# Kernel tuning notes

Measured on AMD Instinct MI355X. Metric: run time of the kernel, lower is better.

## Reference

```python
import jax, jax.numpy as jnp
import numpy as np

N = 32768          # total nodes in batch (M graphs * N_agents)
E = N * 8          # edges (k_neighbors = 8)
DIN = 16           # node_obs_dim
DE = 8             # edge_dim (rel_pos 2 + one-hot 4 + dist 1 + payoff 1)
HE = 128           # embed_hidden_size
C = 64             # TransformerConv out_channels
H = 4              # heads (concat)
HC = H * C         # 256, final node embedding dim
EPS = 1e-5


def _ln(x, g, b):
    m = x.mean(-1, keepdims=True)
    v = ((x - m) ** 2).mean(-1, keepdims=True)
    return (x - m) * jax.lax.rsqrt(v + EPS) * g + b


def _seg_softmax(s, seg, n):
    # numerically stable softmax over edges grouped by destination node
    m = jax.ops.segment_max(s, seg, num_segments=n)
    e = jnp.exp(s - m[seg])
    z = jax.ops.segment_sum(e, seg, num_segments=n)
    return e / z[seg]


def setup_inputs() -> dict:
    key = jax.random.key(0)
    ks = jax.random.split(key, 40)

    def w(i, shape):
        return jax.random.normal(ks[i], shape, jnp.float32) * 0.05

    inp = {
        "x": jax.random.normal(ks[0], (N, DIN), jnp.float32),
        "edge_index": jax.random.randint(ks[1], (2, E), 0, N, dtype=jnp.int32),
        "edge_attr": jax.random.normal(ks[2], (E, DE), jnp.float32),
        # EmbedConv: lin1 + LN + one hidden Linear + LN (embed_layer_N=1)
        "e_W1": w(3, (DIN + DE, HE)), "e_b1": jnp.zeros((HE,), jnp.float32),
        "e_g1": jnp.ones((HE,), jnp.float32), "e_be1": jnp.zeros((HE,), jnp.float32),
        "e_W2": w(4, (HE, HE)), "e_b2": jnp.zeros((HE,), jnp.float32),
        "e_g2": jnp.ones((HE,), jnp.float32), "e_be2": jnp.zeros((HE,), jnp.float32),
    }
    # Two TransformerConv layers; layer0 in=HE, layer1 in=HC (concat heads)
    for l, din in enumerate([HE, HC]):
        base = 5 + l * 6
        inp[f"l{l}_Wq"] = w(base, (din, HC));     inp[f"l{l}_bq"] = jnp.zeros((HC,), jnp.float32)
        inp[f"l{l}_Wk"] = w(base + 1, (din, HC)); inp[f"l{l}_bk"] = jnp.zeros((HC,), jnp.float32)
        inp[f"l{l}_Wv"] = w(base + 2, (din, HC)); inp[f"l{l}_bv"] = jnp.zeros((HC,), jnp.float32)
        inp[f"l{l}_We"] = w(base + 3, (DE, HC))   # lin_edge has no bias in PyG
        inp[f"l{l}_Ws"] = w(base + 4, (din, HC)); inp[f"l{l}_bs"] = jnp.zeros((HC,), jnp.float32)
    return inp


def _tconv(h, edge_attr, src, dst, Wq, bq, Wk, bk, Wv, bv, We, Ws, bs):
    q = (h @ Wq + bq).reshape(N, H, C)
    k = (h @ Wk + bk).reshape(N, H, C)
    v = (h @ Wv + bv).reshape(N, H, C)
    e = (edge_attr @ We).reshape(E, H, C)
    ke = k[src] + e                      # [E,H,C]
    ve = v[src] + e                      # [E,H,C]
    s = (q[dst] * ke).sum(-1) / np.float32(np.sqrt(C))  # [E,H]
    a = _seg_softmax(s, dst, N)          # softmax over in-edges of each dst
    out = jax.ops.segment_sum(a[..., None] * ve, dst, num_segments=N)
    return out.reshape(N, HC) + h @ Ws + bs  # root_weight skip + bias


def reference(x, edge_attr, e_W1, e_b1, e_g1, e_be1, e_W2, e_b2, e_g2, e_be2,
              l0_Wq, l0_bq, l0_Wk, l0_bk, l0_Wv, l0_bv, l0_We, l0_Ws, l0_bs,
              l1_Wq, l1_bq, l1_Wk, l1_bk, l1_Wv, l1_bv, l1_We, l1_Ws, l1_bs,
              edge_index):
    src, dst = edge_index[0], edge_index[1]
    # EmbedConv: per-edge MLP on cat(x_j, edge_attr), scatter-add to dst
    m = jnp.concatenate([x[src], edge_attr], axis=1)    # [E, DIN+DE]
    m = _ln(jax.nn.relu(m @ e_W1 + e_b1), e_g1, e_be1)
    m = _ln(jax.nn.relu(m @ e_W2 + e_b2), e_g2, e_be2)
    h = jax.ops.segment_sum(m, dst, num_segments=N)      # [N, HE]
    # Two TransformerConv layers with ReLU activations
    h = jax.nn.relu(_tconv(h, edge_attr, src, dst, l0_Wq, l0_bq, l0_Wk, l0_bk,
                           l0_Wv, l0_bv, l0_We, l0_Ws, l0_bs))
    h = jax.nn.relu(_tconv(h, edge_attr, src, dst, l1_Wq, l1_bq, l1_Wk, l1_bk,
                           l1_Wv, l1_bv, l1_We, l1_Ws, l1_bs))
    return h  # graph_aggr == 'node': [N, HC]
```

## Files before the change

### kernel.cpp

```cpp
#include <hip/hip_runtime.h>
#include <hip/hip_bf16.h>

#define NN 32768
#define NE 262144

typedef unsigned short u16;
typedef unsigned int   u32;
typedef __bf16 bf16x8 __attribute__((ext_vector_type(8)));
typedef float  f32x16 __attribute__((ext_vector_type(16)));

__device__ __forceinline__ float bf2f(u16 u){ return __uint_as_float(((u32)u)<<16); }
__device__ __forceinline__ u16 f2bf(float f){ __hip_bfloat16 h = __float2bfloat16(f); return *(u16*)&h; }
__device__ __forceinline__ float4 ldbf4(const u16* p){
  ushort4 u = *(const ushort4*)p;
  return make_float4(bf2f(u.x), bf2f(u.y), bf2f(u.z), bf2f(u.w));
}
__device__ __forceinline__ void gload16(const void* g, void* l){
  __builtin_amdgcn_global_load_lds(
      (const __attribute__((address_space(1))) void*)g,
      (__attribute__((address_space(3))) void*)l, 16, 0, 0);
}

__global__ void k_deg(const int* __restrict__ ei, int* deg){
  int e = blockIdx.x*256 + threadIdx.x;
  if (e < NE) atomicAdd(&deg[ei[NE + e]], 1);
}

__global__ void k_scan1(const int* __restrict__ deg, int* __restrict__ rowptr, int* __restrict__ bsum){
  const int t = threadIdx.x, b = blockIdx.x;
  const int i = b*256 + t;
  const int ln = t & 63, wv = t >> 6;
  int v = deg[i];
  #pragma unroll
  for (int d = 1; d < 64; d <<= 1){
    int u = __shfl_up(v, d, 64);
    if (ln >= d) v += u;
  }
  __shared__ int wsum[4];
  if (ln == 63) wsum[wv] = v;
  __syncthreads();
  int p = 0;
  #pragma unroll
  for (int w = 0; w < 4; w++) if (w < wv) p += wsum[w];
  v += p;
  rowptr[i + 1] = v;
  if (t == 255) bsum[b] = v;
}

__global__ void k_scan2(const int* __restrict__ bsum, int* __restrict__ boff){
  const int t = threadIdx.x;
  const int ln = t & 63, wv = t >> 6;
  int own = bsum[t];
  int v = own;
  #pragma unroll
  for (int d = 1; d < 64; d <<= 1){
    int u = __shfl_up(v, d, 64);
    if (ln >= d) v += u;
  }
  __shared__ int wsum[2];
  if (ln == 63) wsum[wv] = v;
  __syncthreads();
  if (wv == 1) v += wsum[0];
  boff[t] = v - own;
}

__global__ void k_scan3(int* __restrict__ rowptr, const int* __restrict__ boff){
  const int t = threadIdx.x, b = blockIdx.x;
  rowptr[1 + b*256 + t] += boff[b];
  if (b == 0 && t == 0) rowptr[0] = 0;
}

__global__ void k_fill(const int* __restrict__ ei, const int* __restrict__ rowptr,
                       int* cursor, const float* __restrict__ ea,
                       int* __restrict__ csrc, float4* __restrict__ ea_csr){
  int e = blockIdx.x*256 + threadIdx.x;
  if (e < NE){
    int d = ei[NE + e];
    int p = rowptr[d] + atomicAdd(&cursor[d], 1);
    csrc[p] = ei[e];
    float4 a = *(const float4*)&ea[(size_t)e*8];
    float4 b = *(const float4*)&ea[(size_t)e*8 + 4];
    ea_csr[(size_t)p*2]     = a;
    ea_csr[(size_t)p*2 + 1] = b;
  }
}

__global__ void k_b2p(const float* __restrict__ W2, const float* __restrict__ be1,
                      const float* __restrict__ b2, float* __restrict__ b2p){
  int f = threadIdx.x;
  float a = b2[f];
  for (int k = 0; k < 128; k++) a += be1[k]*W2[k*128 + f];
  b2p[f] = a;
}

__global__ void k_eprep(const float* __restrict__ W1, const float* __restrict__ b1,
                        const float* __restrict__ W2, const float* __restrict__ g1,
                        const float* __restrict__ b2p, __bf16* __restrict__ Ecat){
  int i = blockIdx.x*256 + threadIdx.x;
  if (i >= 2816) return;
  bf16x8 v;
  if (i < 512){
    int r = i & 31, hh = (i>>5)&1, ks = (i>>6)&1, rt = i>>7;
    int feat = rt*32 + r, k0 = ks*16 + hh*8;
    #pragma unroll
    for (int j = 0; j < 8; j++){
      int k = k0 + j;
      float val = (k < 24) ? W1[k*128 + feat] : ((k == 24) ? b1[feat] : 0.f);
      v[j] = (__bf16)val;
    }
  } else {
    int m = i - 512;
    int r = m & 31, hh = (m>>5)&1, q = m>>6;
    int ks = q % 9, rt = q / 9;
    int feat = rt*32 + r, k0 = ks*16 + hh*8;
    #pragma unroll
    for (int j = 0; j < 8; j++){
      int k = k0 + j;
      float val = (k < 128) ? g1[k]*W2[k*128 + feat] : ((k == 128) ? b2p[feat] : 0.f);
      v[j] = (__bf16)val;
    }
  }
  *(bf16x8*)&Ecat[(size_t)i*8] = v;
}

struct WPtrs { const float* w[8]; const float* b[8]; };

__global__ void k_wprep(WPtrs wp, __bf16* __restrict__ W0cat, __bf16* __restrict__ W1cat,
                        float* __restrict__ bcat0, float* __restrict__ bcat1){
  int gid = blockIdx.x*256 + threadIdx.x;
  if (gid < 16384){
    int mat = gid >> 12, v = gid & 4095;
    int colm = v & 255, q = v >> 8;
    int k0 = (q>>1)*16 + (q&1)*8;
    const float* W = wp.w[mat];
    bf16x8 vec;
    #pragma unroll
    for (int j = 0; j < 8; j++) vec[j] = (__bf16)W[(size_t)(k0+j)*256 + colm];
    *(bf16x8*)&W0cat[((size_t)q*1024 + mat*256 + colm)*8] = vec;
  } else if (gid < 49152){
    int g = gid - 16384;
    int mat = g >> 13, v = g & 8191;
    int colm = v & 255, q = v >> 8;
    int k0 = (q>>1)*16 + (q&1)*8;
    const float* W = wp.w[4+mat];
    bf16x8 vec;
    #pragma unroll
    for (int j = 0; j < 8; j++) vec[j] = (__bf16)W[(size_t)(k0+j)*256 + colm];
    *(bf16x8*)&W1cat[((size_t)q*1024 + mat*256 + colm)*8] = vec;
  } else if (gid < 51200){
    int g = gid - 49152;
    if (g < 1024) bcat0[g] = wp.b[g>>8][g&255];
    else { int h = g-1024; bcat1[h] = wp.b[4 + (h>>8)][h&255]; }
  }
}

__global__ __launch_bounds__(256, 1) void k_embed(
    const float* __restrict__ x, const float4* __restrict__ ea_csr,
    const int* __restrict__ csrc, const int* __restrict__ rowptr,
    const __bf16* __restrict__ Ecat,
    const float* __restrict__ g2, const float* __restrict__ be2,
    u16* __restrict__ h0b)
{
  __shared__ alignas(16) __bf16 sE[2816*8];
  __shared__ float sg2[128], sbe2[128];
  const int t = threadIdx.x;
  const int wv = t >> 6, ln = t & 63, hi = ln >> 5, c32 = ln & 31;

  #pragma unroll
  for (int k = 0; k < 11; k++){
    int base = k*256 + wv*64;
    gload16(Ecat + (size_t)(base + ln)*8, &sE[(size_t)base*8]);
  }
  if (t < 128){ sg2[t] = g2[t]; sbe2[t] = be2[t]; }
  asm volatile("s_waitcnt vmcnt(0)" ::: "memory");
  __syncthreads();

  const int d   = (blockIdx.x*4 + wv)*32 + c32;
  const int rp  = rowptr[d];
  const int deg = rowptr[d+1] - rp;
  int md = deg;
  #pragma unroll
  for (int m = 1; m < 32; m <<= 1) md = max(md, __shfl_xor(md, m, 32));

  f32x16 hacc[4] = {};

  bool vc = deg > 0;
  int p0 = vc ? rp : 0;
  int sc = csrc[p0];
  float4 xa = *(const float4*)&x[(size_t)sc*16 + hi*8];
  float4 xb = *(const float4*)&x[(size_t)sc*16 + hi*8 + 4];
  float4 ga = ea_csr[(size_t)p0*2];
  float4 gb = ea_csr[(size_t)p0*2 + 1];

  for (int j = 0; j < md; j++){
    const float vm = vc ? 1.f : 0.f;
    bf16x8 b1f0, b1f1;
    {
      float xv[8]; *(float4*)&xv[0] = xa; *(float4*)&xv[4] = xb;
      #pragma unroll
      for (int q = 0; q < 8; q++) b1f0[q] = (__bf16)(xv[q]*vm);
      float evv[8]; *(float4*)&evv[0] = ga; *(float4*)&evv[4] = gb;
      #pragma unroll
      for (int q = 0; q < 8; q++)
        b1f1[q] = (__bf16)(hi ? ((q == 0) ? vm : 0.f) : evv[q]*vm);
    }

    bool vn = (j + 1) < deg;
    int pn = vn ? (rp + j + 1) : 0;
    int sn = csrc[pn];
    float4 xan = *(const float4*)&x[(size_t)sn*16 + hi*8];
    float4 xbn = *(const float4*)&x[(size_t)sn*16 + hi*8 + 4];
    float4 gan = ea_csr[(size_t)pn*2];
    float4 gbn = ea_csr[(size_t)pn*2 + 1];

    f32x16 a1[4] = {};
    #pragma unroll
    for (int ks = 0; ks < 2; ks++)
      #pragma unroll
      for (int rt = 0; rt < 4; rt++){
        bf16x8 af = *(const bf16x8*)&sE[((((rt*2 + ks)*2 + hi)*32) + c32)*8];
        a1[rt] = __builtin_amdgcn_mfma_f32_32x32x16_bf16(af, ks ? b1f1 : b1f0, a1[rt], 0, 0, 0);
      }

    {
      float s1 = 0.f, s2 = 0.f;
      #pragma unroll
      for (int rt = 0; rt < 4; rt++)
        #pragma unroll
        for (int rg = 0; rg < 16; rg++){
          float v = fmaxf(a1[rt][rg], 0.f);
          a1[rt][rg] = v; s1 += v; s2 += v*v;
        }
      s1 += __shfl_xor(s1, 32, 64);
      s2 += __shfl_xor(s2, 32, 64);
      float mean = s1*(1.f/128.f);
      float rs = rsqrtf(s2*(1.f/128.f) - mean*mean + 1e-5f);
      #pragma unroll
      for (int rt = 0; rt < 4; rt++)
        #pragma unroll
        for (int rg = 0; rg < 16; rg++)
          a1[rt][rg] = (a1[rt][rg] - mean)*rs;
    }

    f32x16 a2[4] = {};
    #pragma unroll
    for (int ks = 0; ks < 8; ks++){
      const int tt = ks >> 1, bb = (ks & 1)*8;
      float snd[4], rcv[4];
      #pragma unroll
      for (int q = 0; q < 4; q++)
        snd[q] = hi ? a1[tt][bb + q] : a1[tt][bb + 4 + q];
      #pragma unroll
      for (int q = 0; q < 4; q++)
        rcv[q] = __shfl_xor(snd[q], 32, 64);
      bf16x8 bf;
      #pragma unroll
      for (int q = 0; q < 4; q++){
        float lo = hi ? rcv[q] : a1[tt][bb + q];
        float hh = hi ? a1[tt][bb + 4 + q] : rcv[q];
        bf[q]     = (__bf16)lo;
        bf[4 + q] = (__bf16)hh;
      }
      #pragma unroll
      for (int rt = 0; rt < 4; rt++){
        bf16x8 af = *(const bf16x8*)&sE[(512 + (((rt*9 + ks)*2 + hi)*32) + c32)*8];
        a2[rt] = __builtin_amdgcn_mfma_f32_32x32x16_bf16(af, bf, a2[rt], 0, 0, 0);
      }
    }
    {
      bf16x8 bf;
      #pragma unroll
      for (int q = 0; q < 8; q++)
        bf[q] = (__bf16)((!hi && q == 0) ? vm : 0.f);
      #pragma unroll
      for (int rt = 0; rt < 4; rt++){
        bf16x8 af = *(const bf16x8*)&sE[(512 + (((rt*9 + 8)*2 + hi)*32) + c32)*8];
        a2[rt] = __builtin_amdgcn_mfma_f32_32x32x16_bf16(af, bf, a2[rt], 0, 0, 0);
      }
    }

    {
      float s1 = 0.f, s2 = 0.f;
      #pragma unroll
      for (int rt = 0; rt < 4; rt++)
        #pragma unroll
        for (int rg = 0; rg < 16; rg++){
          float v = fmaxf(a2[rt][rg], 0.f);
          a2[rt][rg] = v; s1 += v; s2 += v*v;
        }
      s1 += __shfl_xor(s1, 32, 64);
      s2 += __shfl_xor(s2, 32, 64);
      float mean = s1*(1.f/128.f);
      float rs = rsqrtf(s2*(1.f/128.f) - mean*mean + 1e-5f);
      #pragma unroll
      for (int rt = 0; rt < 4; rt++)
        #pragma unroll
        for (int rg = 0; rg < 16; rg++)
          hacc[rt][rg] += (a2[rt][rg] - mean)*rs;
    }

    vc = vn;
    xa = xan; xb = xbn; ga = gan; gb = gbn;
  }

  const float dd = (float)deg;
  #pragma unroll
  for (int rt = 0; rt < 4; rt++)
    #pragma unroll
    for (int q = 0; q < 4; q++){
      int fb = rt*32 + 8*q + 4*hi;
      ushort4 o;
      o.x = f2bf(sg2[fb+0]*hacc[rt][q*4+0] + dd*sbe2[fb+0]);
      o.y = f2bf(sg2[fb+1]*hacc[rt][q*4+1] + dd*sbe2[fb+1]);
      o.z = f2bf(sg2[fb+2]*hacc[rt][q*4+2] + dd*sbe2[fb+2]);
      o.w = f2bf(sg2[fb+3]*hacc[rt][q*4+3] + dd*sbe2[fb+3]);
      *(ushort4*)&h0b[(size_t)d*128 + fb] = o;
    }
}

template<int K>
__global__ __launch_bounds__(256) void k_qkvs2(const u16* __restrict__ A,
    const __bf16* __restrict__ Wcat, const float* __restrict__ bcat,
    u16* __restrict__ qo, u16* __restrict__ ko, u16* __restrict__ vo, u16* __restrict__ so)
{
  __shared__ alignas(16) __bf16 sA[1024*8];
  __shared__ alignas(16) __bf16 sB[1024*8];
  const int t = threadIdx.x;
  const int swz = (blockIdx.x & 7)*256 + (blockIdx.x >> 3);
  const int r0 = (swz >> 3)*128, c0 = (swz & 7)*128;
  const int wv = t >> 6, ln = t & 63, hi = ln >> 5, c32 = ln & 31;
  const int wr = wv >> 1, wc = wv & 1;

  f32x16 acc[2][2] = {};
  for (int kc = 0; kc < K/64; kc++){
    __syncthreads();
    #pragma unroll
    for (int ii = 0; ii < 4; ii++){
      int v = ii*256 + wv*64 + ln;
      int r = v & 31, hh = (v>>5)&1, ks = (v>>6)&3, rt = v>>8;
      const u16* src = A + (size_t)(r0 + rt*32 + r)*K + kc*64 + ks*16 + hh*8;
      gload16(src, &sA[(size_t)(ii*256 + wv*64)*8]);
    }
    #pragma unroll
    for (int ii = 0; ii < 4; ii++){
      int v = ii*256 + wv*64 + ln;
      int col = v & 127, q = v >> 7;
      const __bf16* src = Wcat + ((size_t)(kc*8 + q)*1024 + c0 + col)*8;
      gload16(src, &sB[(size_t)(ii*256 + wv*64)*8]);
    }
    asm volatile("s_waitcnt vmcnt(0)" ::: "memory");
    __syncthreads();
    #pragma unroll
    for (int ks = 0; ks < 4; ks++){
      bf16x8 af0 = *(const bf16x8*)&sA[((((wr*2+0)*4 + ks)*2 + hi)*32 + c32)*8];
      bf16x8 af1 = *(const bf16x8*)&sA[((((wr*2+1)*4 + ks)*2 + hi)*32 + c32)*8];
      bf16x8 bf0 = *(const bf16x8*)&sB[(((ks*2 + hi)*128) + wc*64 + c32)*8];
      bf16x8 bf1 = *(const bf16x8*)&sB[(((ks*2 + hi)*128) + wc*64 + 32 + c32)*8];
      acc[0][0] = __builtin_amdgcn_mfma_f32_32x32x16_bf16(af0, bf0, acc[0][0], 0, 0, 0);
      acc[0][1] = __builtin_amdgcn_mfma_f32_32x32x16_bf16(af0, bf1, acc[0][1], 0, 0, 0);
      acc[1][0] = __builtin_amdgcn_mfma_f32_32x32x16_bf16(af1, bf0, acc[1][0], 0, 0, 0);
      acc[1][1] = __builtin_amdgcn_mfma_f32_32x32x16_bf16(af1, bf1, acc[1][1], 0, 0, 0);
    }
  }

  u16* om = (c0 < 256) ? qo : (c0 < 512) ? ko : (c0 < 768) ? vo : so;
  const int cb = c0 & 255;
  #pragma unroll
  for (int ci = 0; ci < 2; ci++){
    int colm = cb + wc*64 + ci*32 + c32;
    float bb = bcat[c0 + wc*64 + ci*32 + c32];
    #pragma unroll
    for (int ri = 0; ri < 2; ri++){
      #pragma unroll
      for (int rg = 0; rg < 16; rg++){
        int row = r0 + (wr*2 + ri)*32 + (rg&3) + 8*(rg>>2) + 4*hi;
        om[(size_t)row*256 + colm] = f2bf(acc[ri][ci][rg] + bb);
      }
    }
  }
}

template<bool OBF>
__global__ __launch_bounds__(256) void k_attn(
    const int* __restrict__ csrc, const int* __restrict__ rowptr,
    const float4* __restrict__ ea_csr, const float* __restrict__ We,
    const u16* __restrict__ qb, const u16* __restrict__ kb, const u16* __restrict__ vb,
    const u16* __restrict__ skb, void* __restrict__ outp)
{
  __shared__ float sWe[8*256];
  const int t = threadIdx.x;
  for (int i = t; i < 2048; i += 256) sWe[i] = We[i];
  __syncthreads();

  const int wv = t >> 6, ln = t & 63;
  const int f = (ln >> 4)*64 + (ln & 15)*4;
  const int gw = blockIdx.x*4 + wv, nW = gridDim.x*4;

  for (int d = gw; d < NN; d += nW){
    const int rp = rowptr[d];
    const int dg = rowptr[d+1] - rp;
    float4 qv = ldbf4(qb + (size_t)d*256 + f);
    qv.x *= 0.125f; qv.y *= 0.125f; qv.z *= 0.125f; qv.w *= 0.125f;
    float m = -INFINITY, l = 0.f, o0 = 0, o1 = 0, o2 = 0, o3 = 0;

    if (dg > 0){
      int s0 = csrc[rp];
      float4 ga = ea_csr[(size_t)rp*2];
      float4 gb = ea_csr[(size_t)rp*2 + 1];
      float4 kc = ldbf4(kb + (size_t)s0*256 + f);
      float4 vc = ldbf4(vb + (size_t)s0*256 + f);

      for (int j = 0; j < dg; j++){
        int pn = rp + ((j + 1 < dg) ? (j + 1) : j);
        int sn = csrc[pn];
        float4 gan = ea_csr[(size_t)pn*2];
        float4 gbn = ea_csr[(size_t)pn*2 + 1];
        float4 kn = ldbf4(kb + (size_t)sn*256 + f);
        float4 vn = ldbf4(vb + (size_t)sn*256 + f);

        float eav[8];
        *(float4*)&eav[0] = ga; *(float4*)&eav[4] = gb;
        float e0 = 0, e1 = 0, e2 = 0, e3 = 0;
        #pragma unroll
        for (int i = 0; i < 8; i++){
          float4 w = *(const float4*)&sWe[i*256 + f];
          e0 += eav[i]*w.x; e1 += eav[i]*w.y; e2 += eav[i]*w.z; e3 += eav[i]*w.w;
        }
        float sp = qv.x*(kc.x+e0) + qv.y*(kc.y+e1) + qv.z*(kc.z+e2) + qv.w*(kc.w+e3);
        sp += __shfl_xor(sp, 1, 64); sp += __shfl_xor(sp, 2, 64);
        sp += __shfl_xor(sp, 4, 64); sp += __shfl_xor(sp, 8, 64);
        float nm = fmaxf(m, sp);
        float sc = __expf(m - nm);
        float pp = __expf(sp - nm);
        l = l*sc + pp;
        o0 = o0*sc + pp*(vc.x + e0);
        o1 = o1*sc + pp*(vc.y + e1);
        o2 = o2*sc + pp*(vc.z + e2);
        o3 = o3*sc + pp*(vc.w + e3);
        m = nm;

        kc = kn; vc = vn; ga = gan; gb = gbn;
      }
    }

    float il = (l > 0.f) ? 1.f/l : 0.f;
    float4 sv = ldbf4(skb + (size_t)d*256 + f);
    o0 = fmaxf(o0*il + sv.x, 0.f);
    o1 = fmaxf(o1*il + sv.y, 0.f);
    o2 = fmaxf(o2*il + sv.z, 0.f);
    o3 = fmaxf(o3*il + sv.w, 0.f);
    if constexpr (OBF){
      ushort4 o; o.x = f2bf(o0); o.y = f2bf(o1); o.z = f2bf(o2); o.w = f2bf(o3);
      *(ushort4*)((u16*)outp + (size_t)d*256 + f) = o;
    } else {
      *(float4*)((float*)outp + (size_t)d*256 + f) = make_float4(o0, o1, o2, o3);
    }
  }
}

extern "C" void kernel_launch(void* const* d_in, const int* in_sizes, int n_in,
                              void* d_out, int out_size, void* d_ws, size_t ws_size,
                              hipStream_t stream)
{
  (void)in_sizes; (void)n_in; (void)out_size; (void)ws_size;
  const float* x   = (const float*)d_in[0];
  const int*   ei  = (const int*)  d_in[1];
  const float* ea  = (const float*)d_in[2];
  const float* eW1 = (const float*)d_in[3];
  const float* eb1 = (const float*)d_in[4];
  const float* eg1 = (const float*)d_in[5];
  const float* ebe1= (const float*)d_in[6];
  const float* eW2 = (const float*)d_in[7];
  const float* eb2 = (const float*)d_in[8];
  const float* eg2 = (const float*)d_in[9];
  const float* ebe2= (const float*)d_in[10];

  char* ws = (char*)d_ws;
  const size_t MB = (size_t)1 << 20;
  const size_t KB = (size_t)1 << 10;
  int*   deg    = (int*)(ws);
  int*   cursor = (int*)(ws + 128*KB);
  int*   rowptr = (int*)(ws + 256*KB);
  int*   bsum   = (int*)(ws + 400*KB);
  int*   boff   = (int*)(ws + 402*KB);
  float* b2p    = (float*)(ws + 404*KB);
  int*   csrc   = (int*)(ws + 1*MB);
  float4* ea_csr= (float4*)(ws + 4*MB);
  u16*   qb     = (u16*)(ws + 20*MB);
  u16*   kbuf   = (u16*)(ws + 36*MB);
  u16*   vbuf   = (u16*)(ws + 52*MB);
  u16*   skb    = (u16*)(ws + 68*MB);
  u16*   h1     = (u16*)(ws + 84*MB);
  u16*   h0b    = (u16*)(ws + 100*MB);
  __bf16* W0cat = (__bf16*)(ws + 108*MB);
  __bf16* W1cat = (__bf16*)(ws + 109*MB);
  float* bcat0  = (float*)(ws + 110*MB);
  float* bcat1  = (float*)(ws + 110*MB + 64*KB);
  __bf16* Ecat  = (__bf16*)(ws + 111*MB);

  hipMemsetAsync(deg, 0, 256*KB, stream);

  k_deg  <<<NE/256, 256, 0, stream>>>(ei, deg);
  k_scan1<<<128,    256, 0, stream>>>(deg, rowptr, bsum);
  k_scan2<<<1,      128, 0, stream>>>(bsum, boff);
  k_scan3<<<128,    256, 0, stream>>>(rowptr, boff);
  k_fill <<<NE/256, 256, 0, stream>>>(ei, rowptr, cursor, ea, csrc, ea_csr);
  k_b2p  <<<1,      128, 0, stream>>>(eW2, ebe1, eb2, b2p);
  k_eprep<<<11,     256, 0, stream>>>(eW1, eb1, eW2, eg1, b2p, Ecat);

  WPtrs wp;
  wp.w[0] = (const float*)d_in[11]; wp.b[0] = (const float*)d_in[12];
  wp.w[1] = (const float*)d_in[13]; wp.b[1] = (const float*)d_in[14];
  wp.w[2] = (const float*)d_in[15]; wp.b[2] = (const float*)d_in[16];
  wp.w[3] = (const float*)d_in[18]; wp.b[3] = (const float*)d_in[19];
  wp.w[4] = (const float*)d_in[20]; wp.b[4] = (const float*)d_in[21];
  wp.w[5] = (const float*)d_in[22]; wp.b[5] = (const float*)d_in[23];
  wp.w[6] = (const float*)d_in[24]; wp.b[6] = (const float*)d_in[25];
  wp.w[7] = (const float*)d_in[27]; wp.b[7] = (const float*)d_in[28];
  k_wprep<<<200, 256, 0, stream>>>(wp, W0cat, W1cat, bcat0, bcat1);

  k_embed<<<NN/128, 256, 0, stream>>>(x, ea_csr, csrc, rowptr, Ecat, eg2, ebe2, h0b);

  k_qkvs2<128><<<2048, 256, 0, stream>>>(h0b, W0cat, bcat0, qb, kbuf, vbuf, skb);
  k_attn<true><<<NN/4, 256, 0, stream>>>(csrc, rowptr, ea_csr, (const float*)d_in[17],
                                         qb, kbuf, vbuf, skb, (void*)h1);
  k_qkvs2<256><<<2048, 256, 0, stream>>>(h1, W1cat, bcat1, qb, kbuf, vbuf, skb);
  k_attn<false><<<NN/4, 256, 0, stream>>>(csrc, rowptr, ea_csr, (const float*)d_in[26],
                                          qb, kbuf, vbuf, skb, d_out);
}
```

Before: 335.8 us.

## Refactor attention edge term algebraically and batch-prefetch neighbor indices

The per-edge projection of edge attributes through We is removed from the inner loop. Per head, q·We is precomputed once per destination, and the softmax-weighted sum of raw edge attributes is accumulated and projected through We once at the end. Neighbor source indices are loaded once per wave and broadcast with shuffles, and prefetching uses two alternating register buffers. This cuts the per-edge FMAs and LDS reads, at the cost of extra shuffles per destination and a larger number of live registers.

```diff
diff --git a/kernel.cpp b/kernel.cpp
--- a/kernel.cpp
+++ b/kernel.cpp
@@ -392,63 +392,84 @@
   for (int i = t; i < 2048; i += 256) sWe[i] = We[i];
   __syncthreads();
 
+  const float* eaf = (const float*)ea_csr;
   const int wv = t >> 6, ln = t & 63;
   const int f = (ln >> 4)*64 + (ln & 15)*4;
+  const int iown = ln & 7;
+  const int gbase = ln & ~15;
   const int gw = blockIdx.x*4 + wv, nW = gridDim.x*4;
+
+#define ATT_PRE(KX, VX, EX, jj) do{                                        \
+      int sj_ = ((jj) < 64) ? __shfl(sidx, (jj), 64) : csrc[rp + (jj)];    \
+      KX = ldbf4(kb + (size_t)sj_*256 + f);                                \
+      VX = ldbf4(vb + (size_t)sj_*256 + f);                                \
+      EX = eaf[(size_t)(rp + (jj))*8 + iown];                              \
+    }while(0)
+
+#define ATT_STEP(KX, VX, EX) do{                                           \
+      float spp = qv.x*KX.x + qv.y*KX.y + qv.z*KX.z + qv.w*KX.w;           \
+      spp += EX*wqsel;                                                     \
+      spp += __shfl_xor(spp, 1, 64); spp += __shfl_xor(spp, 2, 64);        \
+      spp += __shfl_xor(spp, 4, 64); spp += __shfl_xor(spp, 8, 64);        \
+      float nm = fmaxf(m, spp);                                            \
+      float sc_ = __expf(m - nm);                                          \
+      float pp = __expf(spp - nm);                                         \
+      l = l*sc_ + pp;                                                      \
+      o0 = o0*sc_ + pp*VX.x; o1 = o1*sc_ + pp*VX.y;                        \
+      o2 = o2*sc_ + pp*VX.z; o3 = o3*sc_ + pp*VX.w;                        \
+      weal = weal*sc_ + pp*EX;                                             \
+      m = nm;                                                              \
+    }while(0)
 
   for (int d = gw; d < NN; d += nW){
     const int rp = rowptr[d];
     const int dg = rowptr[d+1] - rp;
     float4 qv = ldbf4(qb + (size_t)d*256 + f);
     qv.x *= 0.125f; qv.y *= 0.125f; qv.z *= 0.125f; qv.w *= 0.125f;
-    float m = -INFINITY, l = 0.f, o0 = 0, o1 = 0, o2 = 0, o3 = 0;
+    float4 sv = ldbf4(skb + (size_t)d*256 + f);
+
+    float wqsel = 0.f;
+    #pragma unroll
+    for (int i = 0; i < 8; i++){
+      float4 w = *(const float4*)&sWe[i*256 + f];
+      float p = qv.x*w.x + qv.y*w.y + qv.z*w.z + qv.w*w.w;
+      p += __shfl_xor(p, 1, 64); p += __shfl_xor(p, 2, 64);
+      p += __shfl_xor(p, 4, 64); p += __shfl_xor(p, 8, 64);
+      if ((ln & 15) == i) wqsel = p;
+    }
+
+    float m = -INFINITY, l = 0.f, o0 = 0, o1 = 0, o2 = 0, o3 = 0, weal = 0.f;
 
     if (dg > 0){
-      int s0 = csrc[rp];
-      float4 ga = ea_csr[(size_t)rp*2];
-      float4 gb = ea_csr[(size_t)rp*2 + 1];
-      float4 kc = ldbf4(kb + (size_t)s0*256 + f);
-      float4 vc = ldbf4(vb + (size_t)s0*256 + f);
-
-      for (int j = 0; j < dg; j++){
-        int pn = rp + ((j + 1 < dg) ? (j + 1) : j);
-        int sn = csrc[pn];
-        float4 gan = ea_csr[(size_t)pn*2];
-        float4 gbn = ea_csr[(size_t)pn*2 + 1];
-        float4 kn = ldbf4(kb + (size_t)sn*256 + f);
-        float4 vn = ldbf4(vb + (size_t)sn*256 + f);
-
-        float eav[8];
-        *(float4*)&eav[0] = ga; *(float4*)&eav[4] = gb;
-        float e0 = 0, e1 = 0, e2 = 0, e3 = 0;
-        #pragma unroll
-        for (int i = 0; i < 8; i++){
-          float4 w = *(const float4*)&sWe[i*256 + f];
-          e0 += eav[i]*w.x; e1 += eav[i]*w.y; e2 += eav[i]*w.z; e3 += eav[i]*w.w;
-        }
-        float sp = qv.x*(kc.x+e0) + qv.y*(kc.y+e1) + qv.z*(kc.z+e2) + qv.w*(kc.w+e3);
-        sp += __shfl_xor(sp, 1, 64); sp += __shfl_xor(sp, 2, 64);
-        sp += __shfl_xor(sp, 4, 64); sp += __shfl_xor(sp, 8, 64);
-        float nm = fmaxf(m, sp);
-        float sc = __expf(m - nm);
-        float pp = __expf(sp - nm);
-        l = l*sc + pp;
-        o0 = o0*sc + pp*(vc.x + e0);
-        o1 = o1*sc + pp*(vc.y + e1);
-        o2 = o2*sc + pp*(vc.z + e2);
-        o3 = o3*sc + pp*(vc.w + e3);
-        m = nm;
-
-        kc = kn; vc = vn; ga = gan; gb = gbn;
+      int sidx = (ln < dg) ? csrc[rp + ln] : 0;
+      float4 kA, vA, kB, vB; float eA, eB;
+      ATT_PRE(kA, vA, eA, 0);
+      if (dg > 1) ATT_PRE(kB, vB, eB, 1);
+
+      int j = 0;
+      while (j < dg){
+        ATT_STEP(kA, vA, eA);
+        if (j + 2 < dg) ATT_PRE(kA, vA, eA, j + 2);
+        j++;
+        if (j >= dg) break;
+        ATT_STEP(kB, vB, eB);
+        if (j + 2 < dg) ATT_PRE(kB, vB, eB, j + 2);
+        j++;
       }
     }
 
     float il = (l > 0.f) ? 1.f/l : 0.f;
-    float4 sv = ldbf4(skb + (size_t)d*256 + f);
-    o0 = fmaxf(o0*il + sv.x, 0.f);
-    o1 = fmaxf(o1*il + sv.y, 0.f);
-    o2 = fmaxf(o2*il + sv.z, 0.f);
-    o3 = fmaxf(o3*il + sv.w, 0.f);
+    float ec0 = 0, ec1 = 0, ec2 = 0, ec3 = 0;
+    #pragma unroll
+    for (int i = 0; i < 8; i++){
+      float wi = __shfl(weal, gbase + i, 64);
+      float4 w = *(const float4*)&sWe[i*256 + f];
+      ec0 += wi*w.x; ec1 += wi*w.y; ec2 += wi*w.z; ec3 += wi*w.w;
+    }
+    o0 = fmaxf((o0 + ec0)*il + sv.x, 0.f);
+    o1 = fmaxf((o1 + ec1)*il + sv.y, 0.f);
+    o2 = fmaxf((o2 + ec2)*il + sv.z, 0.f);
+    o3 = fmaxf((o3 + ec3)*il + sv.w, 0.f);
     if constexpr (OBF){
       ushort4 o; o.x = f2bf(o0); o.y = f2bf(o1); o.z = f2bf(o2); o.w = f2bf(o3);
       *(ushort4*)((u16*)outp + (size_t)d*256 + f) = o;
@@ -456,6 +477,8 @@
       *(float4*)((float*)outp + (size_t)d*256 + f) = make_float4(o0, o1, o2, o3);
     }
   }
+#undef ATT_PRE
+#undef ATT_STEP
 }
 
 extern "C" void kernel_launch(void* const* d_in, const int* in_sizes, int n_in,
```

Result: no change. 336.8 us (+0.3%).
